# Optimization experiments

Hardware: AMD Instinct MI355X
Metric: run time of the kernel (lower is better)

Reference implementation:

```python
import jax, jax.numpy as jnp
import numpy as np

T, B = 50, 1024
DETER, STOC, EMB, ACT, MLP = 600, 32, 1024, 6, 600
MIN_STD = 0.1

def _p(key, shape):
    return jax.random.normal(key, shape, dtype=jnp.float32) * 0.02

def setup_inputs() -> dict:
    key = jax.random.key(0)
    ks = jax.random.split(key, 20)
    return {
        'actions': jax.random.normal(ks[0], (T, B, ACT), dtype=jnp.float32),
        'nonterminals': jnp.ones((T, B, 1), dtype=jnp.float32),
        'obs_embeddings': jax.random.normal(ks[1], (T, B, EMB), dtype=jnp.float32),
        'noise_prior': jax.random.uniform(ks[2], (T, B, STOC), dtype=jnp.float32),
        'noise_post': jax.random.uniform(ks[3], (T, B, STOC), dtype=jnp.float32),
        'init_deter': jnp.zeros((B, DETER), dtype=jnp.float32),
        'init_stoc': jnp.zeros((B, STOC), dtype=jnp.float32),
        # fc_input: Linear(stoc+action -> deter)
        'W_in': _p(ks[4], (DETER, STOC + ACT)), 'b_in': jnp.zeros((DETER,), jnp.float32),
        # GRUCell(deter, deter): torch layout [3*H, in]
        'W_ih': _p(ks[5], (3 * DETER, DETER)), 'b_ih': jnp.zeros((3 * DETER,), jnp.float32),
        'W_hh': _p(ks[6], (3 * DETER, DETER)), 'b_hh': jnp.zeros((3 * DETER,), jnp.float32),
        # fc_prior: deter -> mlp -> 2*stoc
        'Wp1': _p(ks[7], (MLP, DETER)), 'bp1': jnp.zeros((MLP,), jnp.float32),
        'Wp2': _p(ks[8], (2 * STOC, MLP)), 'bp2': jnp.zeros((2 * STOC,), jnp.float32),
        # fc_posterior: deter+emb -> mlp -> 2*stoc
        'Wq1': _p(ks[9], (MLP, DETER + EMB)), 'bq1': jnp.zeros((MLP,), jnp.float32),
        'Wq2': _p(ks[10], (2 * STOC, MLP)), 'bq2': jnp.zeros((2 * STOC,), jnp.float32),
    }

def _rollout(actions, nonterminals, obs_embeddings, noise_prior, noise_post,
             init_deter, init_stoc, W_in, b_in, W_ih, b_ih, W_hh, b_hh,
             Wp1, bp1, Wp2, bp2, Wq1, bq1, Wq2, bq2):
    def step(carry, inp):
        deter, stoc = carry
        a, nt, emb, n_p, n_q = inp
        # fc_input + ELU
        x = jax.nn.elu(jnp.concatenate([stoc * nt, a], axis=-1) @ W_in.T + b_in)
        # torch GRUCell
        gi = x @ W_ih.T + b_ih            # [B, 3D]
        gh = deter @ W_hh.T + b_hh        # [B, 3D]
        ir, iz, inn = jnp.split(gi, 3, axis=-1)
        hr, hz, hn = jnp.split(gh, 3, axis=-1)
        r = jax.nn.sigmoid(ir + hr)
        z = jax.nn.sigmoid(iz + hz)
        n = jnp.tanh(inn + r * hn)
        h = (1.0 - z) * n + z * deter
        # prior head
        pp = jax.nn.elu(h @ Wp1.T + bp1) @ Wp2.T + bp2
        p_mu, p_std = jnp.split(pp, 2, axis=-1)
        p_std = jax.nn.softplus(p_std) + MIN_STD
        p_stoc = p_mu + p_std * n_p  # uniform noise, matching torch.rand_like
        # posterior head
        qq = jax.nn.elu(jnp.concatenate([h, emb], axis=-1) @ Wq1.T + bq1) @ Wq2.T + bq2
        q_mu, q_std = jnp.split(qq, 2, axis=-1)
        q_std = jax.nn.softplus(q_std) + MIN_STD
        q_stoc = q_mu + q_std * n_q
        out = jnp.concatenate([h, p_mu, p_std, p_stoc, q_mu, q_std, q_stoc], axis=-1)
        return (h, q_stoc), out

    _, outs = jax.lax.scan(step, (init_deter, init_stoc),
                           (actions, nonterminals, obs_embeddings, noise_prior, noise_post))
    return outs  # [T, B, DETER + 6*STOC]

def reference(actions, nonterminals, obs_embeddings, noise_prior, noise_post,
              init_deter, init_stoc, W_in, b_in, W_ih, b_ih, W_hh, b_hh,
              Wp1, bp1, Wp2, bp2, Wq1, bq1, Wq2, bq2):
    return _rollout(actions, nonterminals, obs_embeddings, noise_prior, noise_post,
                    init_deter, init_stoc, W_in, b_in, W_ih, b_ih, W_hh, b_hh,
                    Wp1, bp1, Wp2, bp2, Wq1, bq1, Wq2, bq2)
```

## Files before the change

kernel.cpp:

```cpp
#include <hip/hip_runtime.h>

typedef __bf16 bf16x8 __attribute__((ext_vector_type(8)));
typedef float f32x4 __attribute__((ext_vector_type(4)));
typedef unsigned short u16;
typedef unsigned int u32;
typedef unsigned long long u64;

#define NT 50
#define NB 1024
#define DET 600
#define DP 608
#define NP 640
#define EMB 1024
#define OUTW 792

__device__ __forceinline__ u16 f2bf(float f) {
  unsigned u = __float_as_uint(f);
  u += 0x7FFFu + ((u >> 16) & 1u);
  return (u16)(u >> 16);
}
__device__ __forceinline__ float bf2f(u16 h) { return __uint_as_float(((unsigned)h) << 16); }
__device__ __forceinline__ float eluf(float x) { return x > 0.f ? x : expm1f(x); }
__device__ __forceinline__ float sigm(float x) { return 1.f / (1.f + expf(-x)); }
__device__ __forceinline__ float softplusf(float x) {
  return fmaxf(x, 0.f) + log1pf(expf(-fabsf(x)));
}

__device__ __forceinline__ void gll16(const void* g, void* l) {
  __builtin_amdgcn_global_load_lds(
      (const __attribute__((address_space(1))) u32*)g,
      (__attribute__((address_space(3))) u32*)l, 16, 0, 0);
}


struct GruP {
  const u16* xb; const u16* hb; const u16* W6;
  const float* b_ih; const float* b_hh;
  const float* dprev; int dstride;
  float* out_t; u16* hbn;
};

__global__ __launch_bounds__(256, 2) void gru_k(GruP p)
{
  __shared__ u16 lds[2][8][64 * 32];
  const int tid = threadIdx.x;
  const int lane = tid & 63, w = tid >> 6;
  const int wr = w >> 1, wc = w & 1;
  const int m0 = blockIdx.y * 64, n0 = blockIdx.x * 64;
  const int r16 = lane & 15, k8g = lane >> 4;
  f32x4 acc[6][2][2] = {};

  const int srow = tid >> 2;
  const int sk8 = ((tid & 3) - ((tid >> 3) & 3)) & 3;
  const u16* ax = p.xb + (size_t)(m0 + srow) * DP + sk8 * 8;
  const u16* ah = p.hb + (size_t)(m0 + srow) * DP + sk8 * 8;
  const u16* bw[6];
#pragma unroll
  for (int s = 0; s < 6; s++)
    bw[s] = p.W6 + (size_t)s * NP * DP + (size_t)(n0 + srow) * DP + sk8 * 8;
  const int lo = w * 1024;

  auto stage = [&](int buf, int kc) {
    gll16(ax + kc, (char*)lds[buf][0] + lo);
    gll16(ah + kc, (char*)lds[buf][1] + lo);
#pragma unroll
    for (int s = 0; s < 6; s++) gll16(bw[s] + kc, (char*)lds[buf][2 + s] + lo);
  };
  auto compute = [&](int buf) {
    bf16x8 ax_[2], ah_[2];
#pragma unroll
    for (int i = 0; i < 2; i++) {
      int row = wr * 32 + i * 16 + r16;
      int S = row * 4 + ((k8g + (row >> 1)) & 3);
      ax_[i] = *(const bf16x8*)((const char*)lds[buf][0] + S * 16);
      ah_[i] = *(const bf16x8*)((const char*)lds[buf][1] + S * 16);
    }
#pragma unroll
    for (int s = 0; s < 6; s++) {
#pragma unroll
      for (int j = 0; j < 2; j++) {
        int row = wc * 32 + j * 16 + r16;
        int S = row * 4 + ((k8g + (row >> 1)) & 3);
        bf16x8 b = *(const bf16x8*)((const char*)lds[buf][2 + s] + S * 16);
#pragma unroll
        for (int i = 0; i < 2; i++)
          acc[s][i][j] = __builtin_amdgcn_mfma_f32_16x16x32_bf16(
              (s < 3) ? ax_[i] : ah_[i], b, acc[s][i][j], 0, 0, 0);
      }
    }
  };

  stage(0, 0);
  __syncthreads();
  for (int it = 0; it < 19; ++it) {
    if (it + 1 < 19) stage((it + 1) & 1, (it + 1) * 32);
    compute(it & 1);
    __syncthreads();
  }

#pragma unroll
  for (int j = 0; j < 2; j++) {
    int n = n0 + wc * 32 + j * 16 + r16;
    if (n >= DET) {
      if (n < DP) {
#pragma unroll
        for (int i = 0; i < 2; i++) {
          int mb = m0 + wr * 32 + i * 16 + k8g * 4;
#pragma unroll
          for (int r = 0; r < 4; r++) p.hbn[(size_t)(mb + r) * DP + n] = 0;
        }
      }
      continue;
    }
    float bihr = p.b_ih[n], bihz = p.b_ih[600 + n], bihn = p.b_ih[1200 + n];
    float bhhr = p.b_hh[n], bhhz = p.b_hh[600 + n], bhhn = p.b_hh[1200 + n];
#pragma unroll
    for (int i = 0; i < 2; i++) {
      int mb = m0 + wr * 32 + i * 16 + k8g * 4;
#pragma unroll
      for (int r = 0; r < 4; r++) {
        int m = mb + r;
        float rg = sigm(acc[0][i][j][r] + bihr + acc[3][i][j][r] + bhhr);
        float zg = sigm(acc[1][i][j][r] + bihz + acc[4][i][j][r] + bhhz);
        float ng = tanhf(acc[2][i][j][r] + bihn + rg * (acc[5][i][j][r] + bhhn));
        float h = (1.f - zg) * ng + zg * p.dprev[(size_t)m * p.dstride + n];
        p.out_t[(size_t)m * OUTW + n] = h;
        p.hbn[(size_t)m * DP + n] = f2bf(h);
      }
    }
  }
}

struct GemmZ {
  const u16* A; int lda;
  const u16* A2; int lda2;
  int ksplit;
  const u16* B; int ldb;
  int K;
  const float* bias;
  const u16* Cadd; int ldadd;
  u16* C; int ldc;
  int mode;
};

__global__ __launch_bounds__(256, 2) void gemmP(GemmZ g0, GemmZ g1)
{
  GemmZ g = blockIdx.z ? g1 : g0;
  __shared__ u16 lA[2][128 * 32];
  __shared__ u16 lB[2][128 * 32];
  const int tid = threadIdx.x, lane = tid & 63, w = tid >> 6;
  const int wr = w >> 1, wc = w & 1;
  const size_t m0 = (size_t)blockIdx.y * 128;
  const int n0 = blockIdx.x * 128;
  const int r16 = lane & 15, k8g = lane >> 4;
  f32x4 acc[4][4] = {};

  const int S0 = tid, S1 = tid + 256;
  const int ar0 = S0 >> 2, ak0 = (((S0 & 3) - ((S0 >> 3) & 3)) & 3) * 8;
  const int ar1 = S1 >> 2, ak1 = (((S1 & 3) - ((S1 >> 3) & 3)) & 3) * 8;
  const int lo = w * 1024;
  const int niter = g.K / 32;

  auto stage = [&](int buf, int kc) {
    {
      int kk = kc + ak0;
      const u16* s = (kk < g.ksplit) ? g.A + (m0 + ar0) * (size_t)g.lda + kk
                                     : g.A2 + (m0 + ar0) * (size_t)g.lda2 + (kk - g.ksplit);
      gll16(s, (char*)lA[buf] + lo);
    }
    {
      int kk = kc + ak1;
      const u16* s = (kk < g.ksplit) ? g.A + (m0 + ar1) * (size_t)g.lda + kk
                                     : g.A2 + (m0 + ar1) * (size_t)g.lda2 + (kk - g.ksplit);
      gll16(s, (char*)lA[buf] + 4096 + lo);
    }
    gll16(g.B + (size_t)(n0 + ar0) * g.ldb + kc + ak0, (char*)lB[buf] + lo);
    gll16(g.B + (size_t)(n0 + ar1) * g.ldb + kc + ak1, (char*)lB[buf] + 4096 + lo);
  };
  auto compute = [&](int buf) {
    bf16x8 fa[4], fb[4];
#pragma unroll
    for (int i = 0; i < 4; i++) {
      int row = wr * 64 + i * 16 + r16;
      int S = row * 4 + ((k8g + (row >> 1)) & 3);
      fa[i] = *(const bf16x8*)((const char*)lA[buf] + S * 16);
    }
#pragma unroll
    for (int j = 0; j < 4; j++) {
      int row = wc * 64 + j * 16 + r16;
      int S = row * 4 + ((k8g + (row >> 1)) & 3);
      fb[j] = *(const bf16x8*)((const char*)lB[buf] + S * 16);
    }
#pragma unroll
    for (int i = 0; i < 4; i++)
#pragma unroll
      for (int j = 0; j < 4; j++)
        acc[i][j] = __builtin_amdgcn_mfma_f32_16x16x32_bf16(fa[i], fb[j], acc[i][j], 0, 0, 0);
  };

  stage(0, 0);
  __syncthreads();
  for (int it = 0; it < niter; ++it) {
    if (it + 1 < niter) stage((it + 1) & 1, (it + 1) * 32);
    compute(it & 1);
    __syncthreads();
  }

  if (g.mode == 1) {
#pragma unroll
    for (int i = 0; i < 4; i++) {
      size_t mb = m0 + wr * 64 + i * 16 + k8g * 4;
#pragma unroll
      for (int j = 0; j < 4; j++) {
        int n = n0 + wc * 64 + j * 16 + r16;
        if (n >= DP) continue;
        float b = (n < DET && g.bias) ? g.bias[n] : 0.f;
#pragma unroll
        for (int r = 0; r < 4; r++) {
          float v = acc[i][j][r] + b;
          if (g.Cadd) v += bf2f(g.Cadd[(mb + r) * (size_t)g.ldadd + n]);
          g.C[(mb + r) * (size_t)g.ldc + n] = f2bf(eluf(v));
        }
      }
    }
  } else {
#pragma unroll
    for (int i = 0; i < 4; i++) {
      size_t mb = m0 + wr * 64 + i * 16 + k8g * 4;
#pragma unroll
      for (int j = 0; j < 4; j++) {
        int n = n0 + wc * 64 + j * 16 + r16;
        if (n >= g.ldc) continue;
#pragma unroll
        for (int r = 0; r < 4; r++)
          g.C[(mb + r) * (size_t)g.ldc + n] = f2bf(acc[i][j][r]);
      }
    }
  }
}

struct H2P {
  const u16* phb; const u16* qhb; const u16* Wp2; const u16* Wq2;
  const float* bp2; const float* bq2;
  const float* np_t; const float* nq_t;
  float* out_t;
  const float* nt_next; const float* act_next;
  const u16* Winp; const float* b_in; u16* xb;
};

__global__ __launch_bounds__(256) void heads2x_k(H2P p)
{
  __shared__ u16 xin[16 * 64];
  __shared__ float red[2][64][16];
  const int tid = threadIdx.x, lane = tid & 63, w = tid >> 6;
  const int m0 = blockIdx.x * 16;
  const int r16 = lane & 15, k8g = lane >> 4;
  const bool donext = p.nt_next != nullptr;

  if (donext) ((u64*)xin)[tid] = 0ull;

  const int mat = w & 1, half = w >> 1;
  const u16* Ap = mat ? p.qhb : p.phb;
  const u16* Bp = mat ? p.Wq2 : p.Wp2;
  f32x4 acc[4] = {};
  const int kb = half ? 320 : 0, ke = half ? 608 : 320;
  for (int kc = kb; kc < ke; kc += 32) {
    bf16x8 fa = *(const bf16x8*)&Ap[(size_t)(m0 + r16) * DP + kc + k8g * 8];
#pragma unroll
    for (int j = 0; j < 4; j++) {
      bf16x8 fb = *(const bf16x8*)&Bp[(size_t)(j * 16 + r16) * DP + kc + k8g * 8];
      acc[j] = __builtin_amdgcn_mfma_f32_16x16x32_bf16(fa, fb, acc[j], 0, 0, 0);
    }
  }
  if (half) {
#pragma unroll
    for (int j = 0; j < 4; j++) *(f32x4*)&red[mat][lane][j * 4] = acc[j];
  }
  __syncthreads();
  if (!half) {
#pragma unroll
    for (int j = 0; j < 4; j++) acc[j] += *(const f32x4*)&red[mat][lane][j * 4];
    const float* bias = mat ? p.bq2 : p.bp2;
    const float* noise = mat ? p.nq_t : p.np_t;
    const int ob = mat ? 696 : 600;
#pragma unroll
    for (int j = 0; j < 2; j++) {
      int c = j * 16 + r16;
      float bmu = bias[c], bsd = bias[32 + c];
#pragma unroll
      for (int r = 0; r < 4; r++) {
        int m = m0 + k8g * 4 + r;
        float mu = acc[j][r] + bmu;
        float sd = softplusf(acc[j + 2][r] + bsd) + 0.1f;
        float st = mu + sd * noise[(size_t)m * 32 + c];
        float* op = p.out_t + (size_t)m * OUTW + ob;
        op[c] = mu; op[32 + c] = sd; op[64 + c] = st;
        if (mat && donext) xin[(m - m0) * 64 + c] = f2bf(st * p.nt_next[m]);
      }
    }
  } else if (donext && mat) {
#pragma unroll
    for (int rep = 0; rep < 2; rep++) {
      int idx = lane + rep * 64;
      if (idx < 96) {
        int rr = idx / 6, c = idx - rr * 6;
        xin[rr * 64 + 32 + c] = f2bf(p.act_next[(size_t)(m0 + rr) * 6 + c]);
      }
    }
  }
  if (!donext) return;
  __syncthreads();

  f32x4 xc[10] = {};
  const int nb = w * 160;
#pragma unroll
  for (int kc = 0; kc < 64; kc += 32) {
    bf16x8 fa = *(const bf16x8*)&xin[r16 * 64 + kc + k8g * 8];
#pragma unroll
    for (int j = 0; j < 10; j++) {
      bf16x8 fb = *(const bf16x8*)&p.Winp[(size_t)(nb + j * 16 + r16) * 64 + kc + k8g * 8];
      xc[j] = __builtin_amdgcn_mfma_f32_16x16x32_bf16(fa, fb, xc[j], 0, 0, 0);
    }
  }
#pragma unroll
  for (int j = 0; j < 10; j++) {
    int n = nb + j * 16 + r16;
    if (n >= DP) continue;
#pragma unroll
    for (int r = 0; r < 4; r++) {
      int m = m0 + k8g * 4 + r;
      float v = (n < DET) ? eluf(xc[j][r] + p.b_in[n]) : 0.f;
      p.xb[(size_t)m * DP + n] = f2bf(v);
    }
  }
}

__global__ void wconv_k(const float* src, int srows, int scols, int sstride,
                        u16* dst, int drows, int dstride, int c0, int cw)
{
  int idx = blockIdx.x * 256 + threadIdx.x;
  if (idx >= drows * cw) return;
  int r = idx / cw, c = idx - r * cw;
  float v = (r < srows && c < scols) ? src[(size_t)r * sstride + c] : 0.f;
  dst[(size_t)r * dstride + c0 + c] = f2bf(v);
}

__global__ void conv8_k(const float* src, u16* dst, int n8)
{
  int i = blockIdx.x * 256 + threadIdx.x;
  if (i >= n8) return;
  const float4* s = (const float4*)(src + (size_t)i * 8);
  float4 f0 = s[0], f1 = s[1];
  union { u16 h[8]; int4 v; } cv;
  cv.h[0] = f2bf(f0.x); cv.h[1] = f2bf(f0.y); cv.h[2] = f2bf(f0.z); cv.h[3] = f2bf(f0.w);
  cv.h[4] = f2bf(f1.x); cv.h[5] = f2bf(f1.y); cv.h[6] = f2bf(f1.z); cv.h[7] = f2bf(f1.w);
  *(int4*)(dst + (size_t)i * 8) = cv.v;
}

__global__ void xin0_k(const float* stoc0, const float* nt0, const float* act0, u16* xing)
{
  int i = blockIdx.x * 256 + threadIdx.x;
  if (i >= NB * 64) return;
  int m = i >> 6, c = i & 63;
  float v = 0.f;
  if (c < 32) v = stoc0[m * 32 + c] * nt0[m];
  else if (c < 38) v = act0[m * 6 + (c - 32)];
  xing[i] = f2bf(v);
}

extern "C" void kernel_launch(void* const* d_in, const int* in_sizes, int n_in,
                              void* d_out, int out_size, void* d_ws, size_t ws_size,
                              hipStream_t stream)
{
  const float* actions    = (const float*)d_in[0];
  const float* nonterm    = (const float*)d_in[1];
  const float* emb        = (const float*)d_in[2];
  const float* noise_p    = (const float*)d_in[3];
  const float* noise_q    = (const float*)d_in[4];
  const float* init_deter = (const float*)d_in[5];
  const float* init_stoc  = (const float*)d_in[6];
  const float* W_in = (const float*)d_in[7];
  const float* b_in = (const float*)d_in[8];
  const float* W_ih = (const float*)d_in[9];
  const float* b_ih = (const float*)d_in[10];
  const float* W_hh = (const float*)d_in[11];
  const float* b_hh = (const float*)d_in[12];
  const float* Wp1 = (const float*)d_in[13];
  const float* bp1 = (const float*)d_in[14];
  const float* Wp2 = (const float*)d_in[15];
  const float* bp2 = (const float*)d_in[16];
  const float* Wq1 = (const float*)d_in[17];
  const float* bq1 = (const float*)d_in[18];
  const float* Wq2 = (const float*)d_in[19];
  const float* bq2 = (const float*)d_in[20];
  float* out = (float*)d_out;

  char* wsp = (char*)d_ws;
  size_t o = 0;
  auto alloc = [&](size_t b) { char* p = wsp + o; o = (o + b + 255) & ~(size_t)255; return p; };
  u16* W6   = (u16*)alloc(6ull * NP * DP * 2);
  u16* Wp1p = (u16*)alloc((size_t)NP * DP * 2);
  u16* Wq1h = (u16*)alloc((size_t)NP * DP * 2);
  u16* Wq1f = (u16*)alloc((size_t)NP * 1632 * 2);
  u16* Wq1e = (u16*)alloc((size_t)NP * EMB * 2);
  u16* Wp2p = (u16*)alloc(64ull * DP * 2);
  u16* Wq2p = (u16*)alloc(64ull * DP * 2);
  u16* Winp = (u16*)alloc((size_t)NP * 64 * 2);
  u16* xb   = (u16*)alloc((size_t)NB * DP * 2);
  u16* hb0  = (u16*)alloc((size_t)NB * DP * 2);
  u16* hb1  = (u16*)alloc((size_t)NB * DP * 2);
  u16* phb  = (u16*)alloc((size_t)NB * DP * 2);
  u16* qhb  = (u16*)alloc((size_t)NB * DP * 2);
  u16* xing = (u16*)alloc((size_t)NB * 64 * 2);
  u16* embt = (u16*)alloc((size_t)NB * EMB * 2);
  size_t small_o = o;
  u16* embb = (u16*)alloc((size_t)NT * NB * EMB * 2);
  u16* QE   = (u16*)alloc((size_t)NT * NB * NP * 2);
  const bool bigws = (o <= ws_size);
  if (small_o > ws_size) return;

  auto wcl = [&](const float* src, int sr, int sc, int ss, u16* dst, int dr, int ds, int c0, int cw) {
    int n = dr * cw;
    wconv_k<<<(n + 255) / 256, 256, 0, stream>>>(src, sr, sc, ss, dst, dr, ds, c0, cw);
  };
  for (int s = 0; s < 3; s++) {
    wcl(W_ih + (size_t)s * 600 * 600, 600, 600, 600, W6 + (size_t)s * NP * DP, NP, DP, 0, DP);
    wcl(W_hh + (size_t)s * 600 * 600, 600, 600, 600, W6 + (size_t)(3 + s) * NP * DP, NP, DP, 0, DP);
  }
  wcl(Wp1, 600, 600, 600, Wp1p, NP, DP, 0, DP);
  wcl(Wp2, 64, 600, 600, Wp2p, 64, DP, 0, DP);
  wcl(Wq2, 64, 600, 600, Wq2p, 64, DP, 0, DP);
  wcl(W_in, 600, 38, 38, Winp, NP, 64, 0, 64);
  wcl(init_deter, 1024, 600, 600, hb0, 1024, DP, 0, DP);
  if (bigws) {
    wcl(Wq1, 600, 600, 1624, Wq1h, NP, DP, 0, DP);
    wcl(Wq1 + 600, 600, 1024, 1624, Wq1e, NP, EMB, 0, EMB);
    int n8 = NT * NB * EMB / 8;
    conv8_k<<<(n8 + 255) / 256, 256, 0, stream>>>(emb, embb, n8);
    GemmZ gq = { embb, EMB, nullptr, 0, 1024, Wq1e, EMB, 1024,
                 nullptr, nullptr, 0, QE, NP, 2 };
    gemmP<<<dim3(5, 400, 1), 256, 0, stream>>>(gq, gq);
  } else {
    wcl(Wq1, 600, 600, 1624, Wq1f, NP, 1632, 0, DP);
    wcl(Wq1 + 600, 600, 1024, 1624, Wq1f, NP, 1632, DP, EMB);
  }

  xin0_k<<<NB * 64 / 256, 256, 0, stream>>>(init_stoc, nonterm, actions, xing);
  {
    GemmZ gx = { xing, 64, nullptr, 0, 64, Winp, 64, 64, b_in, nullptr, 0, xb, DP, 1 };
    gemmP<<<dim3(5, 8, 1), 256, 0, stream>>>(gx, gx);
  }

  for (int t = 0; t < NT; t++) {
    float* out_t = out + (size_t)t * NB * OUTW;
    u16* hcur = (t & 1) ? hb1 : hb0;
    u16* hnxt = (t & 1) ? hb0 : hb1;
    const float* dprev = (t == 0) ? init_deter : out + (size_t)(t - 1) * NB * OUTW;
    int dstr = (t == 0) ? 600 : OUTW;

    GruP gp = { xb, hcur, W6, b_ih, b_hh, dprev, dstr, out_t, hnxt };
    gru_k<<<dim3(10, 16, 1), 256, 0, stream>>>(gp);

    GemmZ h0 = { hnxt, DP, nullptr, 0, DP, Wp1p, DP, DP, bp1, nullptr, 0, phb, DP, 1 };
    GemmZ h1;
    if (bigws) {
      h1 = GemmZ{ hnxt, DP, nullptr, 0, DP, Wq1h, DP, DP, bq1,
                  QE + (size_t)t * NB * NP, NP, qhb, DP, 1 };
    } else {
      int n8 = NB * EMB / 8;
      conv8_k<<<(n8 + 255) / 256, 256, 0, stream>>>(emb + (size_t)t * NB * EMB, embt, n8);
      h1 = GemmZ{ hnxt, DP, embt, EMB, DP, Wq1f, 1632, 1632, bq1,
                  nullptr, 0, qhb, DP, 1 };
    }
    gemmP<<<dim3(5, 8, 2), 256, 0, stream>>>(h0, h1);

    H2P hp = { phb, qhb, Wp2p, Wq2p, bp2, bq2,
               noise_p + (size_t)t * NB * 32, noise_q + (size_t)t * NB * 32, out_t,
               (t + 1 < NT) ? nonterm + (size_t)(t + 1) * NB : nullptr,
               (t + 1 < NT) ? actions + (size_t)(t + 1) * NB * 6 : nullptr,
               Winp, b_in, xb };
    heads2x_k<<<64, 256, 0, stream>>>(hp);
  }
}
```

Measured before the change: 4.607 ms.

## Fuse per-timestep kernels into a persistent kernel with grid barriers

Replaces the 150 per-timestep launches (GRU, hidden-layer GEMMs, heads) with one persistent kernel of 160 blocks that loops over all timesteps and synchronises with an atomic grid barrier. The prior/posterior first-layer GEMM, second layer and next-step input projection are fused into a single phase per 16-row slice, so the intermediate activations stay in shared memory instead of being written to global buffers. This removes kernel launch overhead and global round trips. In exchange the second phase uses only 128 blocks with small tiles, and correctness depends on all 160 blocks being co-resident for the spin barrier. The small-workspace fallback path is also dropped.

```diff
diff --git a/kernel.cpp b/kernel.cpp
--- a/kernel.cpp
+++ b/kernel.cpp
@@ -13,6 +13,7 @@
 #define NP 640
 #define EMB 1024
 #define OUTW 792
+#define GBLK 160
 
 __device__ __forceinline__ u16 f2bf(float f) {
   unsigned u = __float_as_uint(f);
@@ -32,120 +33,289 @@
       (__attribute__((address_space(3))) u32*)l, 16, 0, 0);
 }
 
-
-struct GruP {
-  const u16* xb; const u16* hb; const u16* W6;
-  const float* b_ih; const float* b_hh;
-  const float* dprev; int dstride;
-  float* out_t; u16* hbn;
+__device__ __forceinline__ void gridbar(u32* bar, u32 target) {
+  __syncthreads();
+  if (threadIdx.x == 0) {
+    __threadfence();
+    u32 arrived = __hip_atomic_fetch_add(&bar[0], 1u, __ATOMIC_ACQ_REL, __HIP_MEMORY_SCOPE_AGENT);
+    if (arrived == GBLK - 1) {
+      __hip_atomic_store(&bar[0], 0u, __ATOMIC_RELAXED, __HIP_MEMORY_SCOPE_AGENT);
+      __hip_atomic_store(&bar[1], target, __ATOMIC_RELEASE, __HIP_MEMORY_SCOPE_AGENT);
+    } else {
+      while (__hip_atomic_load(&bar[1], __ATOMIC_ACQUIRE, __HIP_MEMORY_SCOPE_AGENT) < target)
+        __builtin_amdgcn_s_sleep(2);
+    }
+    __threadfence();
+  }
+  __syncthreads();
+}
+
+
+struct PK {
+  const u16 *W6, *Wp1, *Wq1h, *Wp2, *Wq2, *Winp, *QE;
+  const float *b_ih, *b_hh, *bp1, *bq1, *bp2, *bq2, *b_in;
+  const float *init_deter, *actions, *nonterm, *noise_p, *noise_q;
+  u16 *xb, *hb0, *hb1;
+  float *out;
+  u32 *bar;
 };
 
-__global__ __launch_bounds__(256, 2) void gru_k(GruP p)
+__global__ __launch_bounds__(256, 1) void rssm_persist(PK p)
 {
-  __shared__ u16 lds[2][8][64 * 32];
-  const int tid = threadIdx.x;
+  __shared__ char smem[65536] __attribute__((aligned(16)));
+
+  const int bid = blockIdx.x, tid = threadIdx.x;
   const int lane = tid & 63, w = tid >> 6;
+  const int r16 = lane & 15, k8g = lane >> 4;
+
+  int my, nx;
+  if (bid < 128) { my = bid >> 3; nx = bid & 7; }
+  else           { my = (bid - 128) >> 1; nx = 8 + (bid & 1); }
+  const int Am0 = my * 64, An0 = nx * 64;
   const int wr = w >> 1, wc = w & 1;
-  const int m0 = blockIdx.y * 64, n0 = blockIdx.x * 64;
-  const int r16 = lane & 15, k8g = lane >> 4;
-  f32x4 acc[6][2][2] = {};
-
   const int srow = tid >> 2;
   const int sk8 = ((tid & 3) - ((tid >> 3) & 3)) & 3;
-  const u16* ax = p.xb + (size_t)(m0 + srow) * DP + sk8 * 8;
-  const u16* ah = p.hb + (size_t)(m0 + srow) * DP + sk8 * 8;
+  const int lo = w * 1024;
   const u16* bw[6];
 #pragma unroll
   for (int s = 0; s < 6; s++)
-    bw[s] = p.W6 + (size_t)s * NP * DP + (size_t)(n0 + srow) * DP + sk8 * 8;
-  const int lo = w * 1024;
-
-  auto stage = [&](int buf, int kc) {
-    gll16(ax + kc, (char*)lds[buf][0] + lo);
-    gll16(ah + kc, (char*)lds[buf][1] + lo);
-#pragma unroll
-    for (int s = 0; s < 6; s++) gll16(bw[s] + kc, (char*)lds[buf][2 + s] + lo);
-  };
-  auto compute = [&](int buf) {
-    bf16x8 ax_[2], ah_[2];
-#pragma unroll
-    for (int i = 0; i < 2; i++) {
-      int row = wr * 32 + i * 16 + r16;
-      int S = row * 4 + ((k8g + (row >> 1)) & 3);
-      ax_[i] = *(const bf16x8*)((const char*)lds[buf][0] + S * 16);
-      ah_[i] = *(const bf16x8*)((const char*)lds[buf][1] + S * 16);
+    bw[s] = p.W6 + (size_t)s * NP * DP + (size_t)(An0 + srow) * DP + sk8 * 8;
+  const u16* axp = p.xb + (size_t)(Am0 + srow) * DP + sk8 * 8;
+  const size_t ahoff = (size_t)(Am0 + srow) * DP + sk8 * 8;
+
+  const bool doB = bid < 128;
+  const int slice = bid >> 1, head = bid & 1;
+  const int Bm0 = slice * 16;
+  const u16* W1 = head ? p.Wq1h : p.Wp1;
+  const float* b1 = head ? p.bq1 : p.bp1;
+  const u16* W2 = head ? p.Wq2 : p.Wp2;
+  const float* b2 = head ? p.bq2 : p.bp2;
+
+  u16* ph = (u16*)smem;
+  float* red = (float*)(smem + 20992);
+  u16* xin = (u16*)(smem + 33280);
+
+  for (int t = 0; t < NT; ++t) {
+    const u16* hcur = (t & 1) ? p.hb1 : p.hb0;
+    u16* hnxt = (t & 1) ? p.hb0 : p.hb1;
+    float* out_t = p.out + (size_t)t * NB * OUTW;
+
+    {
+      const u16* ahp = hcur + ahoff;
+      auto ldsT = [&](int buf, int tile) -> char* { return smem + buf * 32768 + tile * 4096; };
+      f32x4 acc[6][2][2] = {};
+      auto stage = [&](int buf, int kc) {
+        gll16(axp + kc, ldsT(buf, 0) + lo);
+        gll16(ahp + kc, ldsT(buf, 1) + lo);
+#pragma unroll
+        for (int s = 0; s < 6; s++) gll16(bw[s] + kc, ldsT(buf, 2 + s) + lo);
+      };
+      auto compute = [&](int buf) {
+        bf16x8 ax_[2], ah_[2];
+#pragma unroll
+        for (int i = 0; i < 2; i++) {
+          int row = wr * 32 + i * 16 + r16;
+          int S = row * 4 + ((k8g + (row >> 1)) & 3);
+          ax_[i] = *(const bf16x8*)(ldsT(buf, 0) + S * 16);
+          ah_[i] = *(const bf16x8*)(ldsT(buf, 1) + S * 16);
+        }
+#pragma unroll
+        for (int s = 0; s < 6; s++) {
+#pragma unroll
+          for (int j = 0; j < 2; j++) {
+            int row = wc * 32 + j * 16 + r16;
+            int S = row * 4 + ((k8g + (row >> 1)) & 3);
+            bf16x8 b = *(const bf16x8*)(ldsT(buf, 2 + s) + S * 16);
+#pragma unroll
+            for (int i = 0; i < 2; i++)
+              acc[s][i][j] = __builtin_amdgcn_mfma_f32_16x16x32_bf16(
+                  (s < 3) ? ax_[i] : ah_[i], b, acc[s][i][j], 0, 0, 0);
+          }
+        }
+      };
+      stage(0, 0);
+      __syncthreads();
+      for (int it = 0; it < 19; ++it) {
+        if (it + 1 < 19) stage((it + 1) & 1, (it + 1) * 32);
+        compute(it & 1);
+        __syncthreads();
+      }
+      const float* dprev = t ? (out_t - (size_t)NB * OUTW) : p.init_deter;
+      const int dstr = t ? OUTW : DET;
+#pragma unroll
+      for (int j = 0; j < 2; j++) {
+        int n = An0 + wc * 32 + j * 16 + r16;
+        if (n >= DET) {
+          if (n < DP) {
+#pragma unroll
+            for (int i = 0; i < 2; i++) {
+              int mb = Am0 + wr * 32 + i * 16 + k8g * 4;
+#pragma unroll
+              for (int r = 0; r < 4; r++) hnxt[(size_t)(mb + r) * DP + n] = 0;
+            }
+          }
+          continue;
+        }
+        float bihr = p.b_ih[n], bihz = p.b_ih[600 + n], bihn = p.b_ih[1200 + n];
+        float bhhr = p.b_hh[n], bhhz = p.b_hh[600 + n], bhhn = p.b_hh[1200 + n];
+#pragma unroll
+        for (int i = 0; i < 2; i++) {
+          int mb = Am0 + wr * 32 + i * 16 + k8g * 4;
+#pragma unroll
+          for (int r = 0; r < 4; r++) {
+            int m = mb + r;
+            float rg = sigm(acc[0][i][j][r] + bihr + acc[3][i][j][r] + bhhr);
+            float zg = sigm(acc[1][i][j][r] + bihz + acc[4][i][j][r] + bhhz);
+            float ng = tanhf(acc[2][i][j][r] + bihn + rg * (acc[5][i][j][r] + bhhn));
+            float h = (1.f - zg) * ng + zg * dprev[(size_t)m * dstr + n];
+            out_t[(size_t)m * OUTW + n] = h;
+            hnxt[(size_t)m * DP + n] = f2bf(h);
+          }
+        }
+      }
     }
-#pragma unroll
-    for (int s = 0; s < 6; s++) {
-#pragma unroll
-      for (int j = 0; j < 2; j++) {
-        int row = wc * 32 + j * 16 + r16;
-        int S = row * 4 + ((k8g + (row >> 1)) & 3);
-        bf16x8 b = *(const bf16x8*)((const char*)lds[buf][2 + s] + S * 16);
-#pragma unroll
-        for (int i = 0; i < 2; i++)
-          acc[s][i][j] = __builtin_amdgcn_mfma_f32_16x16x32_bf16(
-              (s < 3) ? ax_[i] : ah_[i], b, acc[s][i][j], 0, 0, 0);
+    gridbar(p.bar, 2 * t + 1);
+
+    if (doB) {
+      const bool donext = (t + 1 < NT);
+      const float* noise = (head ? p.noise_q : p.noise_p) + (size_t)t * NB * 32;
+      f32x4 a1[10] = {};
+#pragma unroll 2
+      for (int kc = 0; kc < DP; kc += 32) {
+        bf16x8 fa = *(const bf16x8*)&hnxt[(size_t)(Bm0 + r16) * DP + kc + k8g * 8];
+#pragma unroll
+        for (int i = 0; i < 10; i++) {
+          int j = w + i * 4;
+          if (j < 38) {
+            bf16x8 fb = *(const bf16x8*)&W1[(size_t)(j * 16 + r16) * DP + kc + k8g * 8];
+            a1[i] = __builtin_amdgcn_mfma_f32_16x16x32_bf16(fa, fb, a1[i], 0, 0, 0);
+          }
+        }
+      }
+      for (int i = tid; i < 320; i += 256) {
+        int r = i / 20, c = i - r * 20;
+        *(u32*)&ph[r * 648 + 608 + 2 * c] = 0;
+      }
+      if (head && donext)
+        for (int i = tid; i < 576; i += 256) ((u32*)xin)[i] = 0;
+#pragma unroll
+      for (int i = 0; i < 10; i++) {
+        int j = w + i * 4;
+        if (j >= 38) break;
+        int n = j * 16 + r16;
+#pragma unroll
+        for (int r = 0; r < 4; r++) {
+          int mrow = k8g * 4 + r, m = Bm0 + mrow;
+          float v = a1[i][r];
+          if (n < DET) {
+            v += b1[n];
+            if (head) v += bf2f(p.QE[((size_t)t * NB + m) * NP + n]);
+            ph[mrow * 648 + n] = f2bf(eluf(v));
+          } else {
+            ph[mrow * 648 + n] = 0;
+          }
+        }
+      }
+      __syncthreads();
+      f32x4 a2[4] = {};
+      {
+        int kc0 = w * 160;
+#pragma unroll
+        for (int ks = 0; ks < 5; ks++) {
+          int kc = kc0 + ks * 32;
+          bf16x8 fa = *(const bf16x8*)&ph[r16 * 648 + kc + k8g * 8];
+#pragma unroll
+          for (int j = 0; j < 4; j++) {
+            bf16x8 fb = *(const bf16x8*)&W2[(size_t)(j * 16 + r16) * NP + kc + k8g * 8];
+            a2[j] = __builtin_amdgcn_mfma_f32_16x16x32_bf16(fa, fb, a2[j], 0, 0, 0);
+          }
+        }
+      }
+      if (w) {
+#pragma unroll
+        for (int j = 0; j < 4; j++)
+#pragma unroll
+          for (int r = 0; r < 4; r++)
+            red[(w - 1) * 1024 + (j * 16 + r16) * 16 + k8g * 4 + r] = a2[j][r];
+      }
+      __syncthreads();
+      if (w == 0) {
+#pragma unroll
+        for (int j = 0; j < 4; j++)
+#pragma unroll
+          for (int r = 0; r < 4; r++) {
+            int c = j * 16 + r16, mr = k8g * 4 + r;
+            a2[j][r] += red[c * 16 + mr] + red[1024 + c * 16 + mr] + red[2048 + c * 16 + mr];
+          }
+        const int ob = head ? 696 : 600;
+        const float* ntn = donext ? p.nonterm + (size_t)(t + 1) * NB : nullptr;
+#pragma unroll
+        for (int j = 0; j < 2; j++) {
+          int c = j * 16 + r16;
+          float bmu = b2[c], bsd = b2[32 + c];
+#pragma unroll
+          for (int r = 0; r < 4; r++) {
+            int mr = k8g * 4 + r, m = Bm0 + mr;
+            float mu = a2[j][r] + bmu;
+            float sd = softplusf(a2[j + 2][r] + bsd) + 0.1f;
+            float st = mu + sd * noise[(size_t)m * 32 + c];
+            float* op = out_t + (size_t)m * OUTW + ob;
+            op[c] = mu; op[32 + c] = sd; op[64 + c] = st;
+            if (head && donext) xin[mr * 72 + c] = f2bf(st * ntn[m]);
+          }
+        }
+      } else if (w == 1 && head && donext) {
+        const float* an = p.actions + (size_t)(t + 1) * NB * 6;
+#pragma unroll
+        for (int rep = 0; rep < 2; rep++) {
+          int idx = lane + rep * 64;
+          if (idx < 96) {
+            int rr = idx / 6, c = idx - rr * 6;
+            xin[rr * 72 + 32 + c] = f2bf(an[(size_t)(Bm0 + rr) * 6 + c]);
+          }
+        }
+      }
+      if (head && donext) {
+        __syncthreads();
+        f32x4 xc[10] = {};
+        const int nb = w * 160;
+#pragma unroll
+        for (int kc = 0; kc < 64; kc += 32) {
+          bf16x8 fa = *(const bf16x8*)&xin[r16 * 72 + kc + k8g * 8];
+#pragma unroll
+          for (int j = 0; j < 10; j++) {
+            bf16x8 fb = *(const bf16x8*)&p.Winp[(size_t)(nb + j * 16 + r16) * 64 + kc + k8g * 8];
+            xc[j] = __builtin_amdgcn_mfma_f32_16x16x32_bf16(fa, fb, xc[j], 0, 0, 0);
+          }
+        }
+#pragma unroll
+        for (int j = 0; j < 10; j++) {
+          int n = nb + j * 16 + r16;
+          if (n >= DP) continue;
+#pragma unroll
+          for (int r = 0; r < 4; r++) {
+            int m = Bm0 + k8g * 4 + r;
+            float v = (n < DET) ? eluf(xc[j][r] + p.b_in[n]) : 0.f;
+            p.xb[(size_t)m * DP + n] = f2bf(v);
+          }
+        }
       }
     }
-  };
-
-  stage(0, 0);
-  __syncthreads();
-  for (int it = 0; it < 19; ++it) {
-    if (it + 1 < 19) stage((it + 1) & 1, (it + 1) * 32);
-    compute(it & 1);
-    __syncthreads();
-  }
-
-#pragma unroll
-  for (int j = 0; j < 2; j++) {
-    int n = n0 + wc * 32 + j * 16 + r16;
-    if (n >= DET) {
-      if (n < DP) {
-#pragma unroll
-        for (int i = 0; i < 2; i++) {
-          int mb = m0 + wr * 32 + i * 16 + k8g * 4;
-#pragma unroll
-          for (int r = 0; r < 4; r++) p.hbn[(size_t)(mb + r) * DP + n] = 0;
-        }
-      }
-      continue;
-    }
-    float bihr = p.b_ih[n], bihz = p.b_ih[600 + n], bihn = p.b_ih[1200 + n];
-    float bhhr = p.b_hh[n], bhhz = p.b_hh[600 + n], bhhn = p.b_hh[1200 + n];
-#pragma unroll
-    for (int i = 0; i < 2; i++) {
-      int mb = m0 + wr * 32 + i * 16 + k8g * 4;
-#pragma unroll
-      for (int r = 0; r < 4; r++) {
-        int m = mb + r;
-        float rg = sigm(acc[0][i][j][r] + bihr + acc[3][i][j][r] + bhhr);
-        float zg = sigm(acc[1][i][j][r] + bihz + acc[4][i][j][r] + bhhz);
-        float ng = tanhf(acc[2][i][j][r] + bihn + rg * (acc[5][i][j][r] + bhhn));
-        float h = (1.f - zg) * ng + zg * p.dprev[(size_t)m * p.dstride + n];
-        p.out_t[(size_t)m * OUTW + n] = h;
-        p.hbn[(size_t)m * DP + n] = f2bf(h);
-      }
-    }
+    gridbar(p.bar, 2 * t + 2);
   }
 }
 
 struct GemmZ {
   const u16* A; int lda;
-  const u16* A2; int lda2;
-  int ksplit;
   const u16* B; int ldb;
   int K;
   const float* bias;
-  const u16* Cadd; int ldadd;
   u16* C; int ldc;
   int mode;
 };
 
-__global__ __launch_bounds__(256, 2) void gemmP(GemmZ g0, GemmZ g1)
+__global__ __launch_bounds__(256, 2) void gemmP(GemmZ g)
 {
-  GemmZ g = blockIdx.z ? g1 : g0;
   __shared__ u16 lA[2][128 * 32];
   __shared__ u16 lB[2][128 * 32];
   const int tid = threadIdx.x, lane = tid & 63, w = tid >> 6;
@@ -162,18 +332,8 @@
   const int niter = g.K / 32;
 
   auto stage = [&](int buf, int kc) {
-    {
-      int kk = kc + ak0;
-      const u16* s = (kk < g.ksplit) ? g.A + (m0 + ar0) * (size_t)g.lda + kk
-                                     : g.A2 + (m0 + ar0) * (size_t)g.lda2 + (kk - g.ksplit);
-      gll16(s, (char*)lA[buf] + lo);
-    }
-    {
-      int kk = kc + ak1;
-      const u16* s = (kk < g.ksplit) ? g.A + (m0 + ar1) * (size_t)g.lda + kk
-                                     : g.A2 + (m0 + ar1) * (size_t)g.lda2 + (kk - g.ksplit);
-      gll16(s, (char*)lA[buf] + 4096 + lo);
-    }
+    gll16(g.A + (m0 + ar0) * (size_t)g.lda + kc + ak0, (char*)lA[buf] + lo);
+    gll16(g.A + (m0 + ar1) * (size_t)g.lda + kc + ak1, (char*)lA[buf] + 4096 + lo);
     gll16(g.B + (size_t)(n0 + ar0) * g.ldb + kc + ak0, (char*)lB[buf] + lo);
     gll16(g.B + (size_t)(n0 + ar1) * g.ldb + kc + ak1, (char*)lB[buf] + 4096 + lo);
   };
@@ -206,131 +366,24 @@
     __syncthreads();
   }
 
-  if (g.mode == 1) {
-#pragma unroll
-    for (int i = 0; i < 4; i++) {
-      size_t mb = m0 + wr * 64 + i * 16 + k8g * 4;
-#pragma unroll
-      for (int j = 0; j < 4; j++) {
-        int n = n0 + wc * 64 + j * 16 + r16;
+#pragma unroll
+  for (int i = 0; i < 4; i++) {
+    size_t mb = m0 + wr * 64 + i * 16 + k8g * 4;
+#pragma unroll
+    for (int j = 0; j < 4; j++) {
+      int n = n0 + wc * 64 + j * 16 + r16;
+      if (g.mode == 1) {
         if (n >= DP) continue;
-        float b = (n < DET && g.bias) ? g.bias[n] : 0.f;
-#pragma unroll
-        for (int r = 0; r < 4; r++) {
-          float v = acc[i][j][r] + b;
-          if (g.Cadd) v += bf2f(g.Cadd[(mb + r) * (size_t)g.ldadd + n]);
-          g.C[(mb + r) * (size_t)g.ldc + n] = f2bf(eluf(v));
-        }
-      }
-    }
-  } else {
-#pragma unroll
-    for (int i = 0; i < 4; i++) {
-      size_t mb = m0 + wr * 64 + i * 16 + k8g * 4;
-#pragma unroll
-      for (int j = 0; j < 4; j++) {
-        int n = n0 + wc * 64 + j * 16 + r16;
+        float b = (n < DET) ? g.bias[n] : 0.f;
+#pragma unroll
+        for (int r = 0; r < 4; r++)
+          g.C[(mb + r) * (size_t)g.ldc + n] = f2bf(eluf(acc[i][j][r] + b));
+      } else {
         if (n >= g.ldc) continue;
 #pragma unroll
         for (int r = 0; r < 4; r++)
           g.C[(mb + r) * (size_t)g.ldc + n] = f2bf(acc[i][j][r]);
       }
-    }
-  }
-}
-
-struct H2P {
-  const u16* phb; const u16* qhb; const u16* Wp2; const u16* Wq2;
-  const float* bp2; const float* bq2;
-  const float* np_t; const float* nq_t;
-  float* out_t;
-  const float* nt_next; const float* act_next;
-  const u16* Winp; const float* b_in; u16* xb;
-};
-
-__global__ __launch_bounds__(256) void heads2x_k(H2P p)
-{
-  __shared__ u16 xin[16 * 64];
-  __shared__ float red[2][64][16];
-  const int tid = threadIdx.x, lane = tid & 63, w = tid >> 6;
-  const int m0 = blockIdx.x * 16;
-  const int r16 = lane & 15, k8g = lane >> 4;
-  const bool donext = p.nt_next != nullptr;
-
-  if (donext) ((u64*)xin)[tid] = 0ull;
-
-  const int mat = w & 1, half = w >> 1;
-  const u16* Ap = mat ? p.qhb : p.phb;
-  const u16* Bp = mat ? p.Wq2 : p.Wp2;
-  f32x4 acc[4] = {};
-  const int kb = half ? 320 : 0, ke = half ? 608 : 320;
-  for (int kc = kb; kc < ke; kc += 32) {
-    bf16x8 fa = *(const bf16x8*)&Ap[(size_t)(m0 + r16) * DP + kc + k8g * 8];
-#pragma unroll
-    for (int j = 0; j < 4; j++) {
-      bf16x8 fb = *(const bf16x8*)&Bp[(size_t)(j * 16 + r16) * DP + kc + k8g * 8];
-      acc[j] = __builtin_amdgcn_mfma_f32_16x16x32_bf16(fa, fb, acc[j], 0, 0, 0);
-    }
-  }
-  if (half) {
-#pragma unroll
-    for (int j = 0; j < 4; j++) *(f32x4*)&red[mat][lane][j * 4] = acc[j];
-  }
-  __syncthreads();
-  if (!half) {
-#pragma unroll
-    for (int j = 0; j < 4; j++) acc[j] += *(const f32x4*)&red[mat][lane][j * 4];
-    const float* bias = mat ? p.bq2 : p.bp2;
-    const float* noise = mat ? p.nq_t : p.np_t;
-    const int ob = mat ? 696 : 600;
-#pragma unroll
-    for (int j = 0; j < 2; j++) {
-      int c = j * 16 + r16;
-      float bmu = bias[c], bsd = bias[32 + c];
-#pragma unroll
-      for (int r = 0; r < 4; r++) {
-        int m = m0 + k8g * 4 + r;
-        float mu = acc[j][r] + bmu;
-        float sd = softplusf(acc[j + 2][r] + bsd) + 0.1f;
-        float st = mu + sd * noise[(size_t)m * 32 + c];
-        float* op = p.out_t + (size_t)m * OUTW + ob;
-        op[c] = mu; op[32 + c] = sd; op[64 + c] = st;
-        if (mat && donext) xin[(m - m0) * 64 + c] = f2bf(st * p.nt_next[m]);
-      }
-    }
-  } else if (donext && mat) {
-#pragma unroll
-    for (int rep = 0; rep < 2; rep++) {
-      int idx = lane + rep * 64;
-      if (idx < 96) {
-        int rr = idx / 6, c = idx - rr * 6;
-        xin[rr * 64 + 32 + c] = f2bf(p.act_next[(size_t)(m0 + rr) * 6 + c]);
-      }
-    }
-  }
-  if (!donext) return;
-  __syncthreads();
-
-  f32x4 xc[10] = {};
-  const int nb = w * 160;
-#pragma unroll
-  for (int kc = 0; kc < 64; kc += 32) {
-    bf16x8 fa = *(const bf16x8*)&xin[r16 * 64 + kc + k8g * 8];
-#pragma unroll
-    for (int j = 0; j < 10; j++) {
-      bf16x8 fb = *(const bf16x8*)&p.Winp[(size_t)(nb + j * 16 + r16) * 64 + kc + k8g * 8];
-      xc[j] = __builtin_amdgcn_mfma_f32_16x16x32_bf16(fa, fb, xc[j], 0, 0, 0);
-    }
-  }
-#pragma unroll
-  for (int j = 0; j < 10; j++) {
-    int n = nb + j * 16 + r16;
-    if (n >= DP) continue;
-#pragma unroll
-    for (int r = 0; r < 4; r++) {
-      int m = m0 + k8g * 4 + r;
-      float v = (n < DET) ? eluf(xc[j][r] + p.b_in[n]) : 0.f;
-      p.xb[(size_t)m * DP + n] = f2bf(v);
     }
   }
 }
@@ -397,27 +450,24 @@
 
   char* wsp = (char*)d_ws;
   size_t o = 0;
-  auto alloc = [&](size_t b) { char* p = wsp + o; o = (o + b + 255) & ~(size_t)255; return p; };
+  auto alloc = [&](size_t b) { char* pp = wsp + o; o = (o + b + 255) & ~(size_t)255; return pp; };
   u16* W6   = (u16*)alloc(6ull * NP * DP * 2);
   u16* Wp1p = (u16*)alloc((size_t)NP * DP * 2);
   u16* Wq1h = (u16*)alloc((size_t)NP * DP * 2);
-  u16* Wq1f = (u16*)alloc((size_t)NP * 1632 * 2);
   u16* Wq1e = (u16*)alloc((size_t)NP * EMB * 2);
-  u16* Wp2p = (u16*)alloc(64ull * DP * 2);
-  u16* Wq2p = (u16*)alloc(64ull * DP * 2);
+  u16* Wp2p = (u16*)alloc(64ull * NP * 2);
+  u16* Wq2p = (u16*)alloc(64ull * NP * 2);
   u16* Winp = (u16*)alloc((size_t)NP * 64 * 2);
   u16* xb   = (u16*)alloc((size_t)NB * DP * 2);
   u16* hb0  = (u16*)alloc((size_t)NB * DP * 2);
   u16* hb1  = (u16*)alloc((size_t)NB * DP * 2);
-  u16* phb  = (u16*)alloc((size_t)NB * DP * 2);
-  u16* qhb  = (u16*)alloc((size_t)NB * DP * 2);
   u16* xing = (u16*)alloc((size_t)NB * 64 * 2);
-  u16* embt = (u16*)alloc((size_t)NB * EMB * 2);
-  size_t small_o = o;
+  u32* barp = (u32*)alloc(256);
   u16* embb = (u16*)alloc((size_t)NT * NB * EMB * 2);
   u16* QE   = (u16*)alloc((size_t)NT * NB * NP * 2);
-  const bool bigws = (o <= ws_size);
-  if (small_o > ws_size) return;
+  if (o > ws_size) return;
+
+  hipMemsetAsync(barp, 0, 256, stream);
 
   auto wcl = [&](const float* src, int sr, int sc, int ss, u16* dst, int dr, int ds, int c0, int cw) {
     int n = dr * cw;
@@ -428,57 +478,28 @@
     wcl(W_hh + (size_t)s * 600 * 600, 600, 600, 600, W6 + (size_t)(3 + s) * NP * DP, NP, DP, 0, DP);
   }
   wcl(Wp1, 600, 600, 600, Wp1p, NP, DP, 0, DP);
-  wcl(Wp2, 64, 600, 600, Wp2p, 64, DP, 0, DP);
-  wcl(Wq2, 64, 600, 600, Wq2p, 64, DP, 0, DP);
+  wcl(Wq1, 600, 600, 1624, Wq1h, NP, DP, 0, DP);
+  wcl(Wq1 + 600, 600, 1024, 1624, Wq1e, NP, EMB, 0, EMB);
+  wcl(Wp2, 64, 600, 600, Wp2p, 64, NP, 0, NP);
+  wcl(Wq2, 64, 600, 600, Wq2p, 64, NP, 0, NP);
   wcl(W_in, 600, 38, 38, Winp, NP, 64, 0, 64);
   wcl(init_deter, 1024, 600, 600, hb0, 1024, DP, 0, DP);
-  if (bigws) {
-    wcl(Wq1, 600, 600, 1624, Wq1h, NP, DP, 0, DP);
-    wcl(Wq1 + 600, 600, 1024, 1624, Wq1e, NP, EMB, 0, EMB);
+
+  {
     int n8 = NT * NB * EMB / 8;
     conv8_k<<<(n8 + 255) / 256, 256, 0, stream>>>(emb, embb, n8);
-    GemmZ gq = { embb, EMB, nullptr, 0, 1024, Wq1e, EMB, 1024,
-                 nullptr, nullptr, 0, QE, NP, 2 };
-    gemmP<<<dim3(5, 400, 1), 256, 0, stream>>>(gq, gq);
-  } else {
-    wcl(Wq1, 600, 600, 1624, Wq1f, NP, 1632, 0, DP);
-    wcl(Wq1 + 600, 600, 1024, 1624, Wq1f, NP, 1632, DP, EMB);
-  }
-
+    GemmZ gq = { embb, EMB, Wq1e, EMB, EMB, nullptr, QE, NP, 2 };
+    gemmP<<<dim3(5, 400, 1), 256, 0, stream>>>(gq);
+  }
   xin0_k<<<NB * 64 / 256, 256, 0, stream>>>(init_stoc, nonterm, actions, xing);
   {
-    GemmZ gx = { xing, 64, nullptr, 0, 64, Winp, 64, 64, b_in, nullptr, 0, xb, DP, 1 };
-    gemmP<<<dim3(5, 8, 1), 256, 0, stream>>>(gx, gx);
-  }
-
-  for (int t = 0; t < NT; t++) {
-    float* out_t = out + (size_t)t * NB * OUTW;
-    u16* hcur = (t & 1) ? hb1 : hb0;
-    u16* hnxt = (t & 1) ? hb0 : hb1;
-    const float* dprev = (t == 0) ? init_deter : out + (size_t)(t - 1) * NB * OUTW;
-    int dstr = (t == 0) ? 600 : OUTW;
-
-    GruP gp = { xb, hcur, W6, b_ih, b_hh, dprev, dstr, out_t, hnxt };
-    gru_k<<<dim3(10, 16, 1), 256, 0, stream>>>(gp);
-
-    GemmZ h0 = { hnxt, DP, nullptr, 0, DP, Wp1p, DP, DP, bp1, nullptr, 0, phb, DP, 1 };
-    GemmZ h1;
-    if (bigws) {
-      h1 = GemmZ{ hnxt, DP, nullptr, 0, DP, Wq1h, DP, DP, bq1,
-                  QE + (size_t)t * NB * NP, NP, qhb, DP, 1 };
-    } else {
-      int n8 = NB * EMB / 8;
-      conv8_k<<<(n8 + 255) / 256, 256, 0, stream>>>(emb + (size_t)t * NB * EMB, embt, n8);
-      h1 = GemmZ{ hnxt, DP, embt, EMB, DP, Wq1f, 1632, 1632, bq1,
-                  nullptr, 0, qhb, DP, 1 };
-    }
-    gemmP<<<dim3(5, 8, 2), 256, 0, stream>>>(h0, h1);
-
-    H2P hp = { phb, qhb, Wp2p, Wq2p, bp2, bq2,
-               noise_p + (size_t)t * NB * 32, noise_q + (size_t)t * NB * 32, out_t,
-               (t + 1 < NT) ? nonterm + (size_t)(t + 1) * NB : nullptr,
-               (t + 1 < NT) ? actions + (size_t)(t + 1) * NB * 6 : nullptr,
-               Winp, b_in, xb };
-    heads2x_k<<<64, 256, 0, stream>>>(hp);
-  }
-}
+    GemmZ gx = { xing, 64, Winp, 64, 64, b_in, xb, DP, 1 };
+    gemmP<<<dim3(5, 8, 1), 256, 0, stream>>>(gx);
+  }
+
+  PK pk = { W6, Wp1p, Wq1h, Wp2p, Wq2p, Winp, QE,
+            b_ih, b_hh, bp1, bq1, bp2, bq2, b_in,
+            init_deter, actions, nonterm, noise_p, noise_q,
+            xb, hb0, hb1, out, barp };
+  rssm_persist<<<GBLK, 256, 0, stream>>>(pk);
+}
```

Result: slower. 8.049 ms (+74.7%).
